# Optimization experiments

Hardware: AMD Instinct MI355X
Metric: run time of the kernel (lower is better)

## Reference

```python
import jax, jax.numpy as jnp
import numpy as np
from jax import lax

WINDOW_SIZES = (7, 15, 31)


def _avg_pool_same(x, k):
    # TF AveragePooling2D with padding='same' excludes padded cells from the
    # average (divides by the count of valid elements in each window).
    sums = lax.reduce_window(x, 0.0, lax.add, (1, k, k, 1), (1, 1, 1, 1), 'SAME')
    ones = jnp.ones((1, x.shape[1], x.shape[2], 1), dtype=x.dtype)
    counts = lax.reduce_window(ones, 0.0, lax.add, (1, k, k, 1), (1, 1, 1, 1), 'SAME')
    return sums / counts


def setup_inputs() -> dict:
    key = jax.random.key(0)
    inputs = jax.random.normal(key, (16, 512, 512, 3), dtype=jnp.float32)
    return {"inputs": inputs}


def reference(inputs) -> jnp.ndarray:
    # [B, n_scales, H, W, C]: (avg_pool_k(x) - x) stacked over window sizes
    deviations = [_avg_pool_same(inputs, k) - inputs for k in WINDOW_SIZES]
    return jnp.stack(deviations, axis=1)
```

## Files before the change

kernel.cpp:

```cpp
#include <hip/hip_runtime.h>
#include <hip/hip_bf16.h>


#define HH 512
#define WW 512
#define ROWF 1536
#define NROWS (16 * HH)
#define PADL 48
#define PADR 48
#define RSTR (PADL + ROWF + PADR)
#define HBLK 32
#define NBLK (HH / HBLK)
#define NB 16

static const size_t I_FLOATS = (size_t)NB * HH * RSTR;
static const size_t T_FLOATS = (size_t)NB * NBLK * RSTR;

__global__ __launch_bounds__(256) void row_prefix_pad(
    const float* __restrict__ x, float* __restrict__ I) {
  const int wave = threadIdx.x >> 6;
  const int lane = threadIdx.x & 63;
  const int row = blockIdx.x * 4 + wave;
  const float4* s4 = (const float4*)(x + (size_t)row * ROWF + lane * 24);

  float v[24];
#pragma unroll
  for (int i = 0; i < 6; ++i) {
    float4 t = s4[i];
    v[4*i] = t.x; v[4*i+1] = t.y; v[4*i+2] = t.z; v[4*i+3] = t.w;
  }
  float tot[3];
#pragma unroll
  for (int c = 0; c < 3; ++c) {
    float run = 0.f;
#pragma unroll
    for (int wl = 0; wl < 8; ++wl) { run += v[wl*3+c]; v[wl*3+c] = run; }
    tot[c] = run;
  }
  float rowtot[3];
#pragma unroll
  for (int c = 0; c < 3; ++c) {
    float t = tot[c];
#pragma unroll
    for (int d = 1; d < 64; d <<= 1) {
      float n = __shfl_up(t, d, 64);
      if (lane >= d) t += n;
    }
    float off = t - tot[c];
#pragma unroll
    for (int wl = 0; wl < 8; ++wl) v[wl*3+c] += off;
    rowtot[c] = __shfl(t, 63, 64);
  }

  float* dst = I + (size_t)row * RSTR;
  float4* d4 = (float4*)(dst + PADL + lane * 24);
#pragma unroll
  for (int i = 0; i < 6; ++i)
    d4[i] = make_float4(v[4*i], v[4*i+1], v[4*i+2], v[4*i+3]);

  if (lane < 12) {
    ((float4*)dst)[lane] = make_float4(0.f, 0.f, 0.f, 0.f);
    float p[4];
#pragma unroll
    for (int j = 0; j < 4; ++j) p[j] = rowtot[(lane * 4 + j) % 3];
    ((float4*)(dst + PADL + ROWF))[lane] = make_float4(p[0], p[1], p[2], p[3]);
  }
}

__global__ __launch_bounds__(256) void col_partial_prefix(
    float* __restrict__ I, float* __restrict__ T) {
  const int j = blockIdx.x * 256 + threadIdx.x;
  if (j >= RSTR / 4) return;
  const int blk = blockIdx.y, b = blockIdx.z;
  float4* base = (float4*)(I + ((size_t)b * HH + blk * HBLK) * RSTR) + j;
  const int st4 = RSTR / 4;

  float4 run = base[0];
#pragma unroll 4
  for (int i = 1; i < HBLK; ++i) {
    float4 nv = base[(size_t)i * st4];
    run.x += nv.x; run.y += nv.y; run.z += nv.z; run.w += nv.w;
    base[(size_t)i * st4] = run;
  }
  ((float4*)(T + ((size_t)b * NBLK + blk) * RSTR))[j] = run;
}

template <bool SUB>
__device__ __forceinline__ void acc_hsum(const float* __restrict__ Rp,
                                         int r3, float4& a) {
  float4 L = *(const float4*)(Rp + r3 - 1);
  float4 H = *(const float4*)(Rp + r3 + 3);
  float4 C = *(const float4*)(Rp - r3 - 3);
  if (!SUB) {
    a.x += L.y - C.x; a.y += L.z - C.y; a.z += L.w - C.z; a.w += H.x - C.w;
  } else {
    a.x -= L.y - C.x; a.y -= L.z - C.y; a.z -= L.w - C.z; a.w -= H.x - C.w;
  }
}

__global__ __launch_bounds__(384) void win_dev_ii(
    const float* __restrict__ x, const float* __restrict__ I,
    const float* __restrict__ T, float* __restrict__ out) {
  const int h = blockIdx.x, b = blockIdx.y;
  const int f = threadIdx.x * 4;
  const float* Ib = I + (size_t)b * HH * RSTR;
  const float* Tb = T + (size_t)b * NBLK * RSTR;
  const float4 xv = *(const float4*)(x + ((size_t)b * HH + h) * ROWF + f);
  float* ob = out + ((size_t)b * 3 * HH + h) * ROWF + f;

  int wj[4];
#pragma unroll
  for (int j = 0; j < 4; ++j) wj[j] = (f + j) / 3;

  const int RADv[3] = {3, 7, 15};
#pragma unroll
  for (int s = 0; s < 3; ++s) {
    const int r = RADv[s], r3 = 3 * r;
    const int rt = min(h + r, HH - 1);
    const int rb = h - r;
    float4 hs = make_float4(0.f, 0.f, 0.f, 0.f);
    acc_hsum<false>(Ib + (size_t)rt * RSTR + PADL + f, r3, hs);
    if (rb >= 1) {
      acc_hsum<true>(Ib + (size_t)(rb - 1) * RSTR + PADL + f, r3, hs);
      const int bt = rt >> 5, bb = (rb - 1) >> 5;
      if (bt != bb)
        acc_hsum<false>(Tb + (size_t)bb * RSTR + PADL + f, r3, hs);
    }
    const int rowcnt = rt - max(rb, 0) + 1;
    const float invrow = __builtin_amdgcn_rcpf((float)rowcnt);
    float hv[4] = {hs.x, hs.y, hs.z, hs.w};
    float xs[4] = {xv.x, xv.y, xv.z, xv.w};
    float rv[4];
#pragma unroll
    for (int j = 0; j < 4; ++j) {
      int cc = min(wj[j] + r, WW - 1) - max(wj[j] - r, 0) + 1;
      rv[j] = hv[j] * (invrow * __builtin_amdgcn_rcpf((float)cc)) - xs[j];
    }
    *(float4*)(ob + (size_t)s * HH * ROWF) =
        make_float4(rv[0], rv[1], rv[2], rv[3]);
  }
}

__global__ __launch_bounds__(256) void row_prefix_kernel(
    const float* __restrict__ x, float* __restrict__ P) {
  const int wave = threadIdx.x >> 6;
  const int lane = threadIdx.x & 63;
  const int row = blockIdx.x * 4 + wave;
  const size_t base = (size_t)row * ROWF + (size_t)lane * 24;
  float v[24];
  const float4* s4 = reinterpret_cast<const float4*>(x + base);
#pragma unroll
  for (int i = 0; i < 6; ++i) {
    float4 t = s4[i];
    v[i*4] = t.x; v[i*4+1] = t.y; v[i*4+2] = t.z; v[i*4+3] = t.w;
  }
  float tot[3];
#pragma unroll
  for (int c = 0; c < 3; ++c) {
    float run = 0.f;
#pragma unroll
    for (int wl = 0; wl < 8; ++wl) { run += v[wl*3+c]; v[wl*3+c] = run; }
    tot[c] = run;
  }
#pragma unroll
  for (int c = 0; c < 3; ++c) {
    float t = tot[c];
#pragma unroll
    for (int d = 1; d < 64; d <<= 1) {
      float n = __shfl_up(t, d, 64);
      if (lane >= d) t += n;
    }
    float off = t - tot[c];
#pragma unroll
    for (int wl = 0; wl < 8; ++wl) v[wl*3+c] += off;
  }
  float4* d4 = reinterpret_cast<float4*>(P + base);
#pragma unroll
  for (int i = 0; i < 6; ++i)
    d4[i] = make_float4(v[i*4], v[i*4+1], v[i*4+2], v[i*4+3]);
}

__global__ __launch_bounds__(256) void window_dev_kernel(
    const float* __restrict__ x, const float* __restrict__ P,
    float* __restrict__ out) {
  const int RAD[3] = {3, 7, 15};
  const int flat = blockIdx.x * 256 + threadIdx.x;
  const int w = flat / 3;
  const int c = flat - w * 3;
  const int b = blockIdx.z;
  const int h0 = blockIdx.y * 64;
  const float* Pb = P + (size_t)b * HH * ROWF;
  const float* xb = x + (size_t)b * HH * ROWF;
  float* ob = out + (size_t)b * 3 * HH * ROWF;
  int ihi[3], ilo[3];
  float mlo[3], invcol[3];
#pragma unroll
  for (int s = 0; s < 3; ++s) {
    const int r = RAD[s];
    int lo = w - r; if (lo < 0) lo = 0;
    int hi = w + r; if (hi > WW - 1) hi = WW - 1;
    invcol[s] = __builtin_amdgcn_rcpf((float)(hi - lo + 1));
    ihi[s] = hi * 3 + c;
    ilo[s] = (lo > 0) ? ((lo - 1) * 3 + c) : c;
    mlo[s] = (lo > 0) ? 1.f : 0.f;
  }
  float S[3];
#pragma unroll
  for (int s = 0; s < 3; ++s) {
    const int r = RAD[s];
    int r0 = h0 - r; if (r0 < 0) r0 = 0;
    int r1 = h0 + r; if (r1 > HH - 1) r1 = HH - 1;
    float acc = 0.f;
    for (int hh = r0; hh <= r1; ++hh) {
      const float* Pr = Pb + (size_t)hh * ROWF;
      acc += Pr[ihi[s]] - mlo[s] * Pr[ilo[s]];
    }
    S[s] = acc;
  }
  for (int h = h0; h < h0 + 64; ++h) {
    const float xvv = xb[(size_t)h * ROWF + flat];
    float invrow[3];
#pragma unroll
    for (int s = 0; s < 3; ++s) {
      const int r = RAD[s];
      int rt = h + r; if (rt > HH - 1) rt = HH - 1;
      int rbv = h - r; if (rbv < 0) rbv = 0;
      invrow[s] = __builtin_amdgcn_rcpf((float)(rt - rbv + 1));
    }
#pragma unroll
    for (int s = 0; s < 3; ++s) {
      const int r = RAD[s];
      const float avg = S[s] * (invrow[s] * invcol[s]);
      ob[((size_t)s * HH + h) * ROWF + flat] = avg - xvv;
      const int add = h + 1 + r;
      const int rem = h - r;
      float d = 0.f;
      if (add < HH) {
        const float* Pr = Pb + (size_t)add * ROWF;
        d += Pr[ihi[s]] - mlo[s] * Pr[ilo[s]];
      }
      if (rem >= 0) {
        const float* Pr = Pb + (size_t)rem * ROWF;
        d -= Pr[ihi[s]] - mlo[s] * Pr[ilo[s]];
      }
      S[s] += d;
    }
  }
}

extern "C" void kernel_launch(void* const* d_in, const int* in_sizes, int n_in,
                              void* d_out, int out_size, void* d_ws, size_t ws_size,
                              hipStream_t stream) {
  const float* x = (const float*)d_in[0];
  float* outp = (float*)d_out;
  const size_t need = (I_FLOATS + T_FLOATS) * sizeof(float);

  if (ws_size >= need) {
    float* I = (float*)d_ws;
    float* T = I + I_FLOATS;
    row_prefix_pad<<<NROWS / 4, 256, 0, stream>>>(x, I);
    dim3 g1b((RSTR / 4 + 255) / 256, NBLK, NB);
    col_partial_prefix<<<g1b, 256, 0, stream>>>(I, T);
    dim3 g2(HH, NB);
    win_dev_ii<<<g2, 384, 0, stream>>>(x, I, T, outp);
  } else {
    float* P = (float*)d_ws;
    row_prefix_kernel<<<NROWS / 4, 256, 0, stream>>>(x, P);
    dim3 grid(ROWF / 256, HH / 64, 16);
    window_dev_kernel<<<grid, 256, 0, stream>>>(x, P, outp);
  }
}
```

Measured before the change: 253.0 us.

## Fuse row and column prefix passes into one block-local kernel

```diff
diff --git a/kernel.cpp b/kernel.cpp
--- a/kernel.cpp
+++ b/kernel.cpp
@@ -16,73 +16,131 @@
 static const size_t I_FLOATS = (size_t)NB * HH * RSTR;
 static const size_t T_FLOATS = (size_t)NB * NBLK * RSTR;
 
-__global__ __launch_bounds__(256) void row_prefix_pad(
-    const float* __restrict__ x, float* __restrict__ I) {
-  const int wave = threadIdx.x >> 6;
+__global__ __launch_bounds__(256) void fused_prefix(
+    const float* __restrict__ x, float* __restrict__ I, float* __restrict__ T) {
+  __shared__ float wtot[4][64][25];
+  const int wv = threadIdx.x >> 6;
   const int lane = threadIdx.x & 63;
-  const int row = blockIdx.x * 4 + wave;
-  const float4* s4 = (const float4*)(x + (size_t)row * ROWF + lane * 24);
-
-  float v[24];
-#pragma unroll
-  for (int i = 0; i < 6; ++i) {
-    float4 t = s4[i];
-    v[4*i] = t.x; v[4*i+1] = t.y; v[4*i+2] = t.z; v[4*i+3] = t.w;
-  }
-  float tot[3];
-#pragma unroll
-  for (int c = 0; c < 3; ++c) {
-    float run = 0.f;
-#pragma unroll
-    for (int wl = 0; wl < 8; ++wl) { run += v[wl*3+c]; v[wl*3+c] = run; }
-    tot[c] = run;
-  }
-  float rowtot[3];
-#pragma unroll
-  for (int c = 0; c < 3; ++c) {
-    float t = tot[c];
-#pragma unroll
-    for (int d = 1; d < 64; d <<= 1) {
-      float n = __shfl_up(t, d, 64);
-      if (lane >= d) t += n;
-    }
-    float off = t - tot[c];
-#pragma unroll
-    for (int wl = 0; wl < 8; ++wl) v[wl*3+c] += off;
-    rowtot[c] = __shfl(t, 63, 64);
-  }
-
-  float* dst = I + (size_t)row * RSTR;
-  float4* d4 = (float4*)(dst + PADL + lane * 24);
-#pragma unroll
-  for (int i = 0; i < 6; ++i)
-    d4[i] = make_float4(v[4*i], v[4*i+1], v[4*i+2], v[4*i+3]);
-
-  if (lane < 12) {
-    ((float4*)dst)[lane] = make_float4(0.f, 0.f, 0.f, 0.f);
-    float p[4];
-#pragma unroll
-    for (int j = 0; j < 4; ++j) p[j] = rowtot[(lane * 4 + j) % 3];
-    ((float4*)(dst + PADL + ROWF))[lane] = make_float4(p[0], p[1], p[2], p[3]);
-  }
-}
-
-__global__ __launch_bounds__(256) void col_partial_prefix(
-    float* __restrict__ I, float* __restrict__ T) {
-  const int j = blockIdx.x * 256 + threadIdx.x;
-  if (j >= RSTR / 4) return;
-  const int blk = blockIdx.y, b = blockIdx.z;
-  float4* base = (float4*)(I + ((size_t)b * HH + blk * HBLK) * RSTR) + j;
-  const int st4 = RSTR / 4;
-
-  float4 run = base[0];
-#pragma unroll 4
-  for (int i = 1; i < HBLK; ++i) {
-    float4 nv = base[(size_t)i * st4];
-    run.x += nv.x; run.y += nv.y; run.z += nv.z; run.w += nv.w;
-    base[(size_t)i * st4] = run;
-  }
-  ((float4*)(T + ((size_t)b * NBLK + blk) * RSTR))[j] = run;
+  const int blk = blockIdx.x;
+  const int b = blockIdx.y;
+  const int row0 = b * HH + blk * HBLK + wv * 8;
+
+  float acc[24];
+#pragma unroll
+  for (int j = 0; j < 24; ++j) acc[j] = 0.f;
+
+  for (int rr = 0; rr < 8; ++rr) {
+    const int row = row0 + rr;
+    const float4* s4 = (const float4*)(x + (size_t)row * ROWF + lane * 24);
+    float v[24];
+#pragma unroll
+    for (int i = 0; i < 6; ++i) {
+      float4 t = s4[i];
+      v[4*i] = t.x; v[4*i+1] = t.y; v[4*i+2] = t.z; v[4*i+3] = t.w;
+    }
+    float tot[3];
+#pragma unroll
+    for (int c = 0; c < 3; ++c) {
+      float run = 0.f;
+#pragma unroll
+      for (int wl = 0; wl < 8; ++wl) { run += v[wl*3+c]; v[wl*3+c] = run; }
+      tot[c] = run;
+    }
+#pragma unroll
+    for (int c = 0; c < 3; ++c) {
+      float t = tot[c];
+#pragma unroll
+      for (int d = 1; d < 64; d <<= 1) {
+        float n = __shfl_up(t, d, 64);
+        if (lane >= d) t += n;
+      }
+      float off = t - tot[c];
+#pragma unroll
+      for (int wl = 0; wl < 8; ++wl) v[wl*3+c] += off;
+    }
+#pragma unroll
+    for (int j = 0; j < 24; ++j) acc[j] += v[j];
+
+    float rp0 = __shfl(acc[21], 63, 64);
+    float rp1 = __shfl(acc[22], 63, 64);
+    float rp2 = __shfl(acc[23], 63, 64);
+
+    float* dst = I + (size_t)row * RSTR;
+    float4* d4 = (float4*)(dst + PADL + lane * 24);
+#pragma unroll
+    for (int i = 0; i < 6; ++i)
+      d4[i] = make_float4(acc[4*i], acc[4*i+1], acc[4*i+2], acc[4*i+3]);
+    if (lane < 12) {
+      ((float4*)dst)[lane] = make_float4(0.f, 0.f, 0.f, 0.f);
+      float rp[3] = {rp0, rp1, rp2};
+      float p[4];
+#pragma unroll
+      for (int j = 0; j < 4; ++j) p[j] = rp[(lane * 4 + j) % 3];
+      ((float4*)(dst + PADL + ROWF))[lane] = make_float4(p[0], p[1], p[2], p[3]);
+    }
+  }
+
+#pragma unroll
+  for (int j = 0; j < 24; ++j) wtot[wv][lane][j] = acc[j];
+  __syncthreads();
+
+  if (wv == 0) {
+    float tt[24];
+#pragma unroll
+    for (int j = 0; j < 24; ++j)
+      tt[j] = wtot[0][lane][j] + wtot[1][lane][j] + wtot[2][lane][j] + wtot[3][lane][j];
+    float* trow = T + ((size_t)b * NBLK + blk) * RSTR;
+    float4* t4 = (float4*)(trow + PADL + lane * 24);
+#pragma unroll
+    for (int i = 0; i < 6; ++i)
+      t4[i] = make_float4(tt[4*i], tt[4*i+1], tt[4*i+2], tt[4*i+3]);
+    if (lane < 12) {
+      ((float4*)trow)[lane] = make_float4(0.f, 0.f, 0.f, 0.f);
+      float tp[3];
+#pragma unroll
+      for (int c = 0; c < 3; ++c)
+        tp[c] = wtot[0][63][21+c] + wtot[1][63][21+c] +
+                wtot[2][63][21+c] + wtot[3][63][21+c];
+      float p[4];
+#pragma unroll
+      for (int j = 0; j < 4; ++j) p[j] = tp[(lane * 4 + j) % 3];
+      ((float4*)(trow + PADL + ROWF))[lane] = make_float4(p[0], p[1], p[2], p[3]);
+    }
+  } else {
+    float off[24];
+#pragma unroll
+    for (int j = 0; j < 24; ++j) {
+      float o = wtot[0][lane][j];
+      if (wv >= 2) o += wtot[1][lane][j];
+      if (wv >= 3) o += wtot[2][lane][j];
+      off[j] = o;
+    }
+    float offp[3];
+#pragma unroll
+    for (int c = 0; c < 3; ++c) {
+      float o = wtot[0][63][21+c];
+      if (wv >= 2) o += wtot[1][63][21+c];
+      if (wv >= 3) o += wtot[2][63][21+c];
+      offp[c] = o;
+    }
+    for (int rr = 0; rr < 8; ++rr) {
+      float* dst = I + (size_t)(row0 + rr) * RSTR;
+      float4* d4 = (float4*)(dst + PADL + lane * 24);
+#pragma unroll
+      for (int i = 0; i < 6; ++i) {
+        float4 t = d4[i];
+        t.x += off[4*i]; t.y += off[4*i+1]; t.z += off[4*i+2]; t.w += off[4*i+3];
+        d4[i] = t;
+      }
+      if (lane < 12) {
+        float4* rp = ((float4*)(dst + PADL + ROWF)) + lane;
+        float4 t = *rp;
+        t.x += offp[(lane*4+0)%3]; t.y += offp[(lane*4+1)%3];
+        t.z += offp[(lane*4+2)%3]; t.w += offp[(lane*4+3)%3];
+        *rp = t;
+      }
+    }
+  }
 }
 
 template <bool SUB>
@@ -101,7 +159,9 @@
 __global__ __launch_bounds__(384) void win_dev_ii(
     const float* __restrict__ x, const float* __restrict__ I,
     const float* __restrict__ T, float* __restrict__ out) {
-  const int h = blockIdx.x, b = blockIdx.y;
+  const int bx = blockIdx.x;
+  const int h = ((bx & 7) << 6) + (bx >> 3);
+  const int b = blockIdx.y;
   const int f = threadIdx.x * 4;
   const float* Ib = I + (size_t)b * HH * RSTR;
   const float* Tb = T + (size_t)b * NBLK * RSTR;
@@ -120,11 +180,14 @@
     const int rb = h - r;
     float4 hs = make_float4(0.f, 0.f, 0.f, 0.f);
     acc_hsum<false>(Ib + (size_t)rt * RSTR + PADL + f, r3, hs);
+    const int bt = rt >> 5;
     if (rb >= 1) {
       acc_hsum<true>(Ib + (size_t)(rb - 1) * RSTR + PADL + f, r3, hs);
-      const int bt = rt >> 5, bb = (rb - 1) >> 5;
-      if (bt != bb)
-        acc_hsum<false>(Tb + (size_t)bb * RSTR + PADL + f, r3, hs);
+      for (int k = (rb - 1) >> 5; k < bt; ++k)
+        acc_hsum<false>(Tb + (size_t)k * RSTR + PADL + f, r3, hs);
+    } else {
+      for (int k = 0; k < bt; ++k)
+        acc_hsum<false>(Tb + (size_t)k * RSTR + PADL + f, r3, hs);
     }
     const int rowcnt = rt - max(rb, 0) + 1;
     const float invrow = __builtin_amdgcn_rcpf((float)rowcnt);
@@ -258,9 +321,8 @@
   if (ws_size >= need) {
     float* I = (float*)d_ws;
     float* T = I + I_FLOATS;
-    row_prefix_pad<<<NROWS / 4, 256, 0, stream>>>(x, I);
-    dim3 g1b((RSTR / 4 + 255) / 256, NBLK, NB);
-    col_partial_prefix<<<g1b, 256, 0, stream>>>(I, T);
+    dim3 g1(NBLK, NB);
+    fused_prefix<<<g1, 256, 0, stream>>>(x, I, T);
     dim3 g2(HH, NB);
     win_dev_ii<<<g2, 384, 0, stream>>>(x, I, T, outp);
   } else {
```

New measurement: 235.0 us. 1.08x faster.
